# Kernel optimization log

Measured on AMD Instinct MI355X. Metric: run time of the kernel, lower is better.

## Reference

```python
import jax, jax.numpy as jnp
import numpy as np

B, N, D, H = 2, 2048, 1024, 16
DH = D // H
MASK_VALUE = -1e7


def setup_inputs() -> dict:
    key = jax.random.key(0)
    ks = jax.random.split(key, 8)
    scale = 0.02
    return {
        "queries": jax.random.normal(ks[0], (B, N, D), dtype=jnp.float32),
        "keys": jax.random.normal(ks[1], (B, N, D), dtype=jnp.float32),
        "values": jax.random.normal(ks[2], (B, N, D), dtype=jnp.float32),
        "valid_len": jax.random.randint(ks[3], (B * H,), 1, N + 1, dtype=jnp.int32),
        "Wq": jax.random.normal(ks[4], (D, D), dtype=jnp.float32) * scale,
        "Wk": jax.random.normal(ks[5], (D, D), dtype=jnp.float32) * scale,
        "Wv": jax.random.normal(ks[6], (D, D), dtype=jnp.float32) * scale,
        "Wo": jax.random.normal(ks[7], (D, D), dtype=jnp.float32) * scale,
    }


def reference(queries, keys, values, valid_len, Wq, Wk, Wv, Wo):
    b, n, d = queries.shape
    h, dh = H, d // H

    def split_heads(x):  # (b, n, d) -> (b, h, n, dh)
        return x.reshape(b, n, h, dh).transpose(0, 2, 1, 3)

    q = split_heads(queries @ Wq)
    k = split_heads(keys @ Wk)
    v = split_heads(values @ Wv)

    # (b, h, nq, nk) full score tensor, as in the original naive bmm path
    scores = jnp.einsum("bhqd,bhkd->bhqk", q, k) / jnp.sqrt(jnp.float32(dh))

    # valid_len is 1-D of length b*h; repeat_interleave over queries means the
    # mask depends only on the key index: keep k < valid_len[bh]
    vl = valid_len.reshape(b, h, 1, 1)
    keep = jnp.arange(n)[None, None, None, :] < vl  # (b, h, 1, nk)
    scores = jnp.where(keep, scores, MASK_VALUE)

    attn = jax.nn.softmax(scores, axis=-1)
    heads = jnp.einsum("bhqk,bhkd->bhqd", attn, v)  # (b, h, n, dh)
    out = heads.transpose(0, 2, 1, 3).reshape(b, n, d) @ Wo
    return out
```

## Files before the change

kernel.cpp:

```cpp
#include <hip/hip_runtime.h>

#define B_ 2
#define N_ 2048
#define D_ 1024
#define H_ 16
#define DH_ 64

typedef _Float16 half8 __attribute__((ext_vector_type(8)));
typedef _Float16 half4 __attribute__((ext_vector_type(4)));
typedef float f32x4 __attribute__((ext_vector_type(4)));

__device__ __forceinline__ void gl2lds16(const _Float16* g, _Float16* l) {
  __builtin_amdgcn_global_load_lds(
      (const __attribute__((address_space(1))) void*)g,
      (__attribute__((address_space(3))) void*)l, 16, 0, 0);
}

__global__ __launch_bounds__(256) void convert_x_kernel(
    const float* __restrict__ q, const float* __restrict__ k,
    const float* __restrict__ v, _Float16* __restrict__ dst) {
  const float* s = (blockIdx.y == 0) ? q : (blockIdx.y == 1) ? k : v;
  _Float16* d = dst + (size_t)blockIdx.y * ((size_t)B_ * N_ * D_);
  size_t idx = ((size_t)blockIdx.x * 256 + threadIdx.x) * 8;
  float4 a = *(const float4*)(s + idx);
  float4 b = *(const float4*)(s + idx + 4);
  half8 h;
  h[0] = (_Float16)a.x; h[1] = (_Float16)a.y; h[2] = (_Float16)a.z; h[3] = (_Float16)a.w;
  h[4] = (_Float16)b.x; h[5] = (_Float16)b.y; h[6] = (_Float16)b.z; h[7] = (_Float16)b.w;
  *(half8*)(d + idx) = h;
}

__global__ __launch_bounds__(256) void convert_w_kernel(
    const float* __restrict__ Wq, const float* __restrict__ Wk,
    const float* __restrict__ Wv, const float* __restrict__ Wo,
    _Float16* __restrict__ WtAll) {
  const float* W = (blockIdx.z == 0) ? Wq : (blockIdx.z == 1) ? Wk
                  : (blockIdx.z == 2) ? Wv : Wo;
  _Float16* Wt = WtAll + (size_t)blockIdx.z * D_ * D_;
  __shared__ float tile[64][65];
  int k0 = blockIdx.y * 64, n0 = blockIdx.x * 64;
  int tr = threadIdx.x >> 4, tc = threadIdx.x & 15;
#pragma unroll
  for (int i = 0; i < 4; ++i) {
    int r = tr + i * 16;
    float4 va = *(const float4*)(W + (size_t)(k0 + r) * D_ + n0 + tc * 4);
    tile[r][tc * 4 + 0] = va.x; tile[r][tc * 4 + 1] = va.y;
    tile[r][tc * 4 + 2] = va.z; tile[r][tc * 4 + 3] = va.w;
  }
  __syncthreads();
#pragma unroll
  for (int i = 0; i < 4; ++i) {
    int r = tr + i * 16;
    half4 hv;
    hv[0] = (_Float16)tile[tc * 4 + 0][r];
    hv[1] = (_Float16)tile[tc * 4 + 1][r];
    hv[2] = (_Float16)tile[tc * 4 + 2][r];
    hv[3] = (_Float16)tile[tc * 4 + 3][r];
    *(half4*)(Wt + (size_t)(n0 + r) * D_ + k0 + tc * 4) = hv;
  }
}

#define BK 32

template <int NT, int MODE>
__global__ __launch_bounds__(256) void gemm_f16_kernel(
    const _Float16* __restrict__ Aall, const _Float16* __restrict__ Btall,
    _Float16* __restrict__ ChAll, float* __restrict__ Cf32) {
  constexpr int BN = NT * 32;
  constexpr int K = D_;
  __shared__ __attribute__((aligned(16))) _Float16 As[128 * BK];
  __shared__ __attribute__((aligned(16))) _Float16 Bs[BN * BK];
  const int z = blockIdx.z;
  const _Float16* A  = Aall  + (size_t)z * ((size_t)B_ * N_ * D_);
  const _Float16* Bt = Btall + (size_t)z * ((size_t)D_ * D_);
  _Float16* Chead = ChAll + (size_t)z * ((size_t)B_ * N_ * D_);

  const int tid = threadIdx.x;
  const int m0 = blockIdx.y * 128, n0 = blockIdx.x * BN;
  const int lane = tid & 63, w = tid >> 6;
  const int quad = lane >> 4, l15 = lane & 15;
  const int wm = (w >> 1) * 64, wn = (w & 1) * (BN / 2);
  const int swz = (quad ^ ((l15 >> 1) & 3)) * 8;
  f32x4 acc[4][NT] = {};

  for (int kt = 0; kt < K; kt += BK) {
    if (kt) __syncthreads();
#pragma unroll
    for (int p = 0; p < 2; ++p) {
      int c = p * 256 + tid;
      int row = c >> 2, pg = c & 3;
      int gl = pg ^ ((row >> 1) & 3);
      gl2lds16(A + (size_t)(m0 + row) * K + kt + gl * 8, &As[c * 8]);
    }
#pragma unroll
    for (int p = 0; p < NT / 2; ++p) {
      int c = p * 256 + tid;
      int row = c >> 2, pg = c & 3;
      int gl = pg ^ ((row >> 1) & 3);
      gl2lds16(Bt + (size_t)(n0 + row) * K + kt + gl * 8, &Bs[c * 8]);
    }
    __syncthreads();
    half8 af[4], bf[NT];
#pragma unroll
    for (int mt = 0; mt < 4; ++mt)
      af[mt] = *(const half8*)&As[(wm + mt * 16 + l15) * 32 + swz];
#pragma unroll
    for (int nt = 0; nt < NT; ++nt)
      bf[nt] = *(const half8*)&Bs[(wn + nt * 16 + l15) * 32 + swz];
#pragma unroll
    for (int mt = 0; mt < 4; ++mt)
#pragma unroll
      for (int nt = 0; nt < NT; ++nt)
        acc[mt][nt] = __builtin_amdgcn_mfma_f32_16x16x32_f16(
            af[mt], bf[nt], acc[mt][nt], 0, 0, 0);
  }

#pragma unroll
  for (int mt = 0; mt < 4; ++mt) {
    int mrow = m0 + wm + mt * 16 + quad * 4;
#pragma unroll
    for (int nt = 0; nt < NT; ++nt) {
      int jcol = n0 + wn + nt * 16 + l15;
#pragma unroll
      for (int r = 0; r < 4; ++r) {
        float val = acc[mt][nt][r];
        int m = mrow + r;
        if (MODE == 0) {
          int b = m >> 11, n = m & (N_ - 1);
          int h = jcol >> 6, dh = jcol & (DH_ - 1);
          Chead[((((size_t)(b * H_ + h)) * N_ + n) * DH_) + dh] = (_Float16)val;
        } else {
          Cf32[(size_t)m * D_ + jcol] = val;
        }
      }
    }
  }
}

__global__ __launch_bounds__(256, 4) void attn_kernel(
    const _Float16* __restrict__ Qh, const _Float16* __restrict__ Kh,
    const _Float16* __restrict__ Vh, const int* __restrict__ vlen,
    _Float16* __restrict__ Hd) {
  __shared__ __attribute__((aligned(16))) _Float16 Ks[2][64 * 64];
  __shared__ __attribute__((aligned(16))) _Float16 Vt[2][64 * 64];
  const int bh = blockIdx.x, q0 = blockIdx.y * 64;
  const int b = bh >> 4, h = bh & (H_ - 1);
  const int vl = vlen[bh];
  const int tid = threadIdx.x, lane = tid & 63, w = tid >> 6;
  const int quad = lane >> 4, l15 = lane & 15;
  const _Float16* Qb = Qh + (size_t)bh * N_ * DH_;
  const _Float16* Kb = Kh + (size_t)bh * N_ * DH_;
  const _Float16* Vb = Vh + (size_t)bh * N_ * DH_;
  const int KT = (vl + 63) >> 6;

  const half8 qb0 = *(const half8*)(Qb + (size_t)(q0 + w * 16 + l15) * DH_ + quad * 8);
  const half8 qb1 = *(const half8*)(Qb + (size_t)(q0 + w * 16 + l15) * DH_ + 32 + quad * 8);

  half8 kpre[2], vpre[2];
  auto prefetch = [&](int k0) {
#pragma unroll
    for (int p = 0; p < 2; ++p) {
      int c = p * 256 + tid;
      int row = c >> 3, pg = c & 7, g = pg ^ (row & 7);
      kpre[p] = *(const half8*)(Kb + (size_t)(k0 + row) * DH_ + g * 8);
      vpre[p] = *(const half8*)(Vb + (size_t)(k0 + lane) * DH_ + (w + p * 4) * 8);
    }
  };
  auto commit = [&](int buf) {
#pragma unroll
    for (int p = 0; p < 2; ++p) {
      int c = p * 256 + tid;
      *(half8*)&Ks[buf][c * 8] = kpre[p];
      int dhg = w + p * 4;
#pragma unroll
      for (int u = 0; u < 8; ++u) {
        int dh = dhg * 8 + u;
        Vt[buf][dh * 64 + (((lane >> 2) ^ (dh & 15)) << 2) + (lane & 3)] = vpre[p][u];
      }
    }
  };

  prefetch(0);
  commit(0);
  if (KT > 1) prefetch(64);
  __syncthreads();

  const int sw  = (quad ^ (l15 & 7)) * 8;
  const int sw2 = ((quad + 4) ^ (l15 & 7)) * 8;
  const float sc2 = 0.125f * 1.44269504088896f;
  const half4 ones = {(_Float16)1, (_Float16)1, (_Float16)1, (_Float16)1};
  f32x4 Oacc[4] = {};
  f32x4 lacc = {};

  for (int kt = 0; kt < KT; ++kt) {
    const int cur = kt & 1;
    if (kt + 1 < KT) commit(1 - cur);
    if (kt + 2 < KT) prefetch((kt + 2) * 64);

    f32x4 s[4];
#pragma unroll
    for (int nt = 0; nt < 4; ++nt) {
      int r = nt * 16 + l15;
      half8 ka0 = *(const half8*)&Ks[cur][r * 64 + sw];
      half8 ka1 = *(const half8*)&Ks[cur][r * 64 + sw2];
      f32x4 c = {};
      c = __builtin_amdgcn_mfma_f32_16x16x32_f16(ka0, qb0, c, 0, 0, 0);
      c = __builtin_amdgcn_mfma_f32_16x16x32_f16(ka1, qb1, c, 0, 0, 0);
      s[nt] = c;
    }
    const int k0 = kt * 64;
    half4 pf[4];
    if (k0 + 64 <= vl) {
#pragma unroll
      for (int nt = 0; nt < 4; ++nt)
#pragma unroll
        for (int r = 0; r < 4; ++r)
          pf[nt][r] = (_Float16)exp2f(s[nt][r] * sc2);
    } else {
#pragma unroll
      for (int nt = 0; nt < 4; ++nt) {
        int keyb = k0 + nt * 16 + quad * 4;
#pragma unroll
        for (int r = 0; r < 4; ++r) {
          float p = exp2f(s[nt][r] * sc2);
          pf[nt][r] = (keyb + r < vl) ? (_Float16)p : (_Float16)0.f;
        }
      }
    }
#pragma unroll
    for (int nt = 0; nt < 4; ++nt) {
      lacc = __builtin_amdgcn_mfma_f32_16x16x16f16(ones, pf[nt], lacc, 0, 0, 0);
#pragma unroll
      for (int dt = 0; dt < 4; ++dt) {
        int dh = dt * 16 + l15;
        half4 va = *(const half4*)&Vt[cur][dh * 64 + (((nt * 4 + quad) ^ l15) << 2)];
        Oacc[dt] = __builtin_amdgcn_mfma_f32_16x16x16f16(va, pf[nt], Oacc[dt], 0, 0, 0);
      }
    }
    __syncthreads();
  }

  float inv_l = 1.0f / lacc[0];
  int q = q0 + w * 16 + l15;
  _Float16* out = Hd + ((size_t)(b * N_ + q)) * D_ + h * DH_;
#pragma unroll
  for (int dt = 0; dt < 4; ++dt) {
    half4 o;
#pragma unroll
    for (int r = 0; r < 4; ++r) o[r] = (_Float16)(Oacc[dt][r] * inv_l);
    *(half4*)(out + dt * 16 + quad * 4) = o;
  }
}

extern "C" void kernel_launch(void* const* d_in, const int* in_sizes, int n_in,
                              void* d_out, int out_size, void* d_ws, size_t ws_size,
                              hipStream_t stream) {
  const float* q  = (const float*)d_in[0];
  const float* k  = (const float*)d_in[1];
  const float* v  = (const float*)d_in[2];
  const int*   vl = (const int*)d_in[3];
  const float* Wq = (const float*)d_in[4];
  const float* Wk = (const float*)d_in[5];
  const float* Wv = (const float*)d_in[6];
  const float* Wo = (const float*)d_in[7];

  const size_t XSZ = (size_t)B_ * N_ * D_;
  const size_t WSZ = (size_t)D_ * D_;
  _Float16* ws = (_Float16*)d_ws;
  _Float16* Xf = ws;
  _Float16* Wt = Xf + 3 * XSZ;
  _Float16* Qh = Wt + 4 * WSZ;
  _Float16* Hd = Qh + 3 * XSZ;

  convert_x_kernel<<<dim3(2048, 3), 256, 0, stream>>>(q, k, v, Xf);
  convert_w_kernel<<<dim3(16, 16, 4), 256, 0, stream>>>(Wq, Wk, Wv, Wo, Wt);

  gemm_f16_kernel<4, 0><<<dim3(D_ / 128, 32, 3), 256, 0, stream>>>(
      Xf, Wt, Qh, nullptr);

  attn_kernel<<<dim3(B_ * H_, N_ / 64), 256, 0, stream>>>(
      Qh, Qh + XSZ, Qh + 2 * XSZ, vl, Hd);

  gemm_f16_kernel<2, 1><<<dim3(D_ / 64, 32, 1), 256, 0, stream>>>(
      Hd, Wt + 3 * WSZ, nullptr, (float*)d_out);
}
```

Baseline: 243.3 us.

## Add persistent LPT-scheduled attention, pre-transposed V, and BK=64 GEMM tiles

Attention becomes a persistent kernel: 512 blocks pull work items from an atomic counter, and heads are ordered longest-valid-length first by a small sort kernel. This aims to balance the uneven per-head work that comes from variable valid_len. A separate kernel pre-transposes V in global memory so the attention LDS commit uses vectorized half4 stores instead of scalar scatter stores. The GEMM K-tile is doubled to 64 with a new XOR swizzle, halving the number of barriers per K loop. The cost is two extra launches, an atomic per work item, and more LDS per GEMM block, which may lower occupancy.

```diff
diff --git a/kernel.cpp b/kernel.cpp
--- a/kernel.cpp
+++ b/kernel.cpp
@@ -5,6 +5,7 @@
 #define D_ 1024
 #define H_ 16
 #define DH_ 64
+#define NITEMS 1024
 
 typedef _Float16 half8 __attribute__((ext_vector_type(8)));
 typedef _Float16 half4 __attribute__((ext_vector_type(4)));
@@ -60,16 +61,14 @@
   }
 }
 
-#define BK 32
-
 template <int NT, int MODE>
 __global__ __launch_bounds__(256) void gemm_f16_kernel(
     const _Float16* __restrict__ Aall, const _Float16* __restrict__ Btall,
     _Float16* __restrict__ ChAll, float* __restrict__ Cf32) {
   constexpr int BN = NT * 32;
   constexpr int K = D_;
-  __shared__ __attribute__((aligned(16))) _Float16 As[128 * BK];
-  __shared__ __attribute__((aligned(16))) _Float16 Bs[BN * BK];
+  __shared__ __attribute__((aligned(16))) _Float16 As[128 * 64];
+  __shared__ __attribute__((aligned(16))) _Float16 Bs[BN * 64];
   const int z = blockIdx.z;
   const _Float16* A  = Aall  + (size_t)z * ((size_t)B_ * N_ * D_);
   const _Float16* Bt = Btall + (size_t)z * ((size_t)D_ * D_);
@@ -80,39 +79,47 @@
   const int lane = tid & 63, w = tid >> 6;
   const int quad = lane >> 4, l15 = lane & 15;
   const int wm = (w >> 1) * 64, wn = (w & 1) * (BN / 2);
-  const int swz = (quad ^ ((l15 >> 1) & 3)) * 8;
+  const int l7 = l15 & 7;
   f32x4 acc[4][NT] = {};
 
-  for (int kt = 0; kt < K; kt += BK) {
+  for (int kt = 0; kt < K; kt += 64) {
     if (kt) __syncthreads();
 #pragma unroll
-    for (int p = 0; p < 2; ++p) {
+    for (int p = 0; p < 4; ++p) {
       int c = p * 256 + tid;
-      int row = c >> 2, pg = c & 3;
-      int gl = pg ^ ((row >> 1) & 3);
+      int row = c >> 3, pg = c & 7, gl = pg ^ (row & 7);
       gl2lds16(A + (size_t)(m0 + row) * K + kt + gl * 8, &As[c * 8]);
     }
 #pragma unroll
-    for (int p = 0; p < NT / 2; ++p) {
+    for (int p = 0; p < NT; ++p) {
       int c = p * 256 + tid;
-      int row = c >> 2, pg = c & 3;
-      int gl = pg ^ ((row >> 1) & 3);
+      int row = c >> 3, pg = c & 7, gl = pg ^ (row & 7);
       gl2lds16(Bt + (size_t)(n0 + row) * K + kt + gl * 8, &Bs[c * 8]);
     }
     __syncthreads();
-    half8 af[4], bf[NT];
-#pragma unroll
-    for (int mt = 0; mt < 4; ++mt)
-      af[mt] = *(const half8*)&As[(wm + mt * 16 + l15) * 32 + swz];
-#pragma unroll
-    for (int nt = 0; nt < NT; ++nt)
-      bf[nt] = *(const half8*)&Bs[(wn + nt * 16 + l15) * 32 + swz];
-#pragma unroll
-    for (int mt = 0; mt < 4; ++mt)
-#pragma unroll
-      for (int nt = 0; nt < NT; ++nt)
-        acc[mt][nt] = __builtin_amdgcn_mfma_f32_16x16x32_f16(
-            af[mt], bf[nt], acc[mt][nt], 0, 0, 0);
+    half8 af[4][2], bf[NT][2];
+#pragma unroll
+    for (int mt = 0; mt < 4; ++mt) {
+      int row = wm + mt * 16 + l15;
+#pragma unroll
+      for (int hh = 0; hh < 2; ++hh)
+        af[mt][hh] = *(const half8*)&As[row * 64 + (((quad + 4 * hh) ^ l7) * 8)];
+    }
+#pragma unroll
+    for (int nt = 0; nt < NT; ++nt) {
+      int row = wn + nt * 16 + l15;
+#pragma unroll
+      for (int hh = 0; hh < 2; ++hh)
+        bf[nt][hh] = *(const half8*)&Bs[row * 64 + (((quad + 4 * hh) ^ l7) * 8)];
+    }
+#pragma unroll
+    for (int hh = 0; hh < 2; ++hh)
+#pragma unroll
+      for (int mt = 0; mt < 4; ++mt)
+#pragma unroll
+        for (int nt = 0; nt < NT; ++nt)
+          acc[mt][nt] = __builtin_amdgcn_mfma_f32_16x16x32_f16(
+              af[mt][hh], bf[nt][hh], acc[mt][nt], 0, 0, 0);
   }
 
 #pragma unroll
@@ -137,118 +144,167 @@
   }
 }
 
+__global__ __launch_bounds__(256) void transpose_v_kernel(
+    const _Float16* __restrict__ Vh, _Float16* __restrict__ VtG) {
+  __shared__ float Ls[64][65];
+  int bh = blockIdx.y, k0 = blockIdx.x * 64;
+  int tid = threadIdx.x;
+  const _Float16* src = Vh + (size_t)bh * N_ * DH_;
+#pragma unroll
+  for (int p = 0; p < 2; ++p) {
+    int c = p * 256 + tid, row = c >> 3, pg = c & 7;
+    half8 hv = *(const half8*)(src + (size_t)(k0 + row) * DH_ + pg * 8);
+#pragma unroll
+    for (int u = 0; u < 8; ++u) Ls[row][pg * 8 + u] = (float)hv[u];
+  }
+  __syncthreads();
+  _Float16* dst = VtG + (size_t)bh * N_ * DH_;
+#pragma unroll
+  for (int p = 0; p < 2; ++p) {
+    int c = p * 256 + tid, dh = c >> 3, pg = c & 7;
+    half8 hv;
+#pragma unroll
+    for (int u = 0; u < 8; ++u) hv[u] = (_Float16)Ls[pg * 8 + u][dh];
+    *(half8*)(dst + (size_t)dh * N_ + k0 + pg * 8) = hv;
+  }
+}
+
+__global__ void sort_heads_kernel(const int* __restrict__ vlen,
+                                  int* __restrict__ order, int* __restrict__ ctr) {
+  int i = threadIdx.x;
+  if (i == 0) *ctr = 0;
+  if (i < B_ * H_) {
+    int vi = vlen[i], rank = 0;
+    for (int j = 0; j < B_ * H_; ++j) {
+      int vj = vlen[j];
+      if (vj > vi || (vj == vi && j < i)) ++rank;
+    }
+    order[rank] = i;
+  }
+}
+
 __global__ __launch_bounds__(256, 4) void attn_kernel(
     const _Float16* __restrict__ Qh, const _Float16* __restrict__ Kh,
-    const _Float16* __restrict__ Vh, const int* __restrict__ vlen,
-    _Float16* __restrict__ Hd) {
+    const _Float16* __restrict__ VtG, const int* __restrict__ vlen,
+    _Float16* __restrict__ Hd, const int* __restrict__ order,
+    int* __restrict__ ctr) {
   __shared__ __attribute__((aligned(16))) _Float16 Ks[2][64 * 64];
   __shared__ __attribute__((aligned(16))) _Float16 Vt[2][64 * 64];
-  const int bh = blockIdx.x, q0 = blockIdx.y * 64;
-  const int b = bh >> 4, h = bh & (H_ - 1);
-  const int vl = vlen[bh];
+  __shared__ int sh_item;
   const int tid = threadIdx.x, lane = tid & 63, w = tid >> 6;
   const int quad = lane >> 4, l15 = lane & 15;
-  const _Float16* Qb = Qh + (size_t)bh * N_ * DH_;
-  const _Float16* Kb = Kh + (size_t)bh * N_ * DH_;
-  const _Float16* Vb = Vh + (size_t)bh * N_ * DH_;
-  const int KT = (vl + 63) >> 6;
-
-  const half8 qb0 = *(const half8*)(Qb + (size_t)(q0 + w * 16 + l15) * DH_ + quad * 8);
-  const half8 qb1 = *(const half8*)(Qb + (size_t)(q0 + w * 16 + l15) * DH_ + 32 + quad * 8);
-
-  half8 kpre[2], vpre[2];
-  auto prefetch = [&](int k0) {
-#pragma unroll
-    for (int p = 0; p < 2; ++p) {
-      int c = p * 256 + tid;
-      int row = c >> 3, pg = c & 7, g = pg ^ (row & 7);
-      kpre[p] = *(const half8*)(Kb + (size_t)(k0 + row) * DH_ + g * 8);
-      vpre[p] = *(const half8*)(Vb + (size_t)(k0 + lane) * DH_ + (w + p * 4) * 8);
-    }
-  };
-  auto commit = [&](int buf) {
-#pragma unroll
-    for (int p = 0; p < 2; ++p) {
-      int c = p * 256 + tid;
-      *(half8*)&Ks[buf][c * 8] = kpre[p];
-      int dhg = w + p * 4;
-#pragma unroll
-      for (int u = 0; u < 8; ++u) {
-        int dh = dhg * 8 + u;
-        Vt[buf][dh * 64 + (((lane >> 2) ^ (dh & 15)) << 2) + (lane & 3)] = vpre[p][u];
-      }
-    }
-  };
-
-  prefetch(0);
-  commit(0);
-  if (KT > 1) prefetch(64);
-  __syncthreads();
-
   const int sw  = (quad ^ (l15 & 7)) * 8;
   const int sw2 = ((quad + 4) ^ (l15 & 7)) * 8;
   const float sc2 = 0.125f * 1.44269504088896f;
   const half4 ones = {(_Float16)1, (_Float16)1, (_Float16)1, (_Float16)1};
-  f32x4 Oacc[4] = {};
-  f32x4 lacc = {};
-
-  for (int kt = 0; kt < KT; ++kt) {
-    const int cur = kt & 1;
-    if (kt + 1 < KT) commit(1 - cur);
-    if (kt + 2 < KT) prefetch((kt + 2) * 64);
-
-    f32x4 s[4];
-#pragma unroll
-    for (int nt = 0; nt < 4; ++nt) {
-      int r = nt * 16 + l15;
-      half8 ka0 = *(const half8*)&Ks[cur][r * 64 + sw];
-      half8 ka1 = *(const half8*)&Ks[cur][r * 64 + sw2];
-      f32x4 c = {};
-      c = __builtin_amdgcn_mfma_f32_16x16x32_f16(ka0, qb0, c, 0, 0, 0);
-      c = __builtin_amdgcn_mfma_f32_16x16x32_f16(ka1, qb1, c, 0, 0, 0);
-      s[nt] = c;
-    }
-    const int k0 = kt * 64;
-    half4 pf[4];
-    if (k0 + 64 <= vl) {
-#pragma unroll
-      for (int nt = 0; nt < 4; ++nt)
-#pragma unroll
-        for (int r = 0; r < 4; ++r)
-          pf[nt][r] = (_Float16)exp2f(s[nt][r] * sc2);
-    } else {
+
+  while (true) {
+    if (tid == 0) sh_item = atomicAdd(ctr, 1);
+    __syncthreads();
+    const int item = sh_item;
+    if (item >= NITEMS) return;
+    const int bh = order[item >> 5];
+    const int q0 = (item & 31) * 64;
+    const int b = bh >> 4, h = bh & (H_ - 1);
+    const int vl = vlen[bh];
+    const int KT = (vl + 63) >> 6;
+    const _Float16* Qb = Qh  + (size_t)bh * N_ * DH_;
+    const _Float16* Kb = Kh  + (size_t)bh * N_ * DH_;
+    const _Float16* Vb = VtG + (size_t)bh * N_ * DH_;
+
+    const half8 qb0 = *(const half8*)(Qb + (size_t)(q0 + w * 16 + l15) * DH_ + quad * 8);
+    const half8 qb1 = *(const half8*)(Qb + (size_t)(q0 + w * 16 + l15) * DH_ + 32 + quad * 8);
+
+    half8 kpre[2], vpre[2];
+    auto prefetch = [&](int k0k) {
+#pragma unroll
+      for (int p = 0; p < 2; ++p) {
+        int c = p * 256 + tid;
+        int row = c >> 3, pg = c & 7;
+        kpre[p] = *(const half8*)(Kb + (size_t)(k0k + row) * DH_ + (pg ^ (row & 7)) * 8);
+        vpre[p] = *(const half8*)(Vb + (size_t)row * N_ + k0k + pg * 8);
+      }
+    };
+    auto commit = [&](int buf) {
+#pragma unroll
+      for (int p = 0; p < 2; ++p) {
+        int c = p * 256 + tid;
+        int row = c >> 3, pg = c & 7;
+        *(half8*)&Ks[buf][c * 8] = kpre[p];
+        int j0 = (pg * 2) ^ (row & 15), j1 = (pg * 2 + 1) ^ (row & 15);
+        half4 lo = {vpre[p][0], vpre[p][1], vpre[p][2], vpre[p][3]};
+        half4 hi = {vpre[p][4], vpre[p][5], vpre[p][6], vpre[p][7]};
+        *(half4*)&Vt[buf][row * 64 + j0 * 4] = lo;
+        *(half4*)&Vt[buf][row * 64 + j1 * 4] = hi;
+      }
+    };
+
+    prefetch(0);
+    commit(0);
+    if (KT > 1) prefetch(64);
+    __syncthreads();
+
+    f32x4 Oacc[4] = {};
+    f32x4 lacc = {};
+
+    for (int kt = 0; kt < KT; ++kt) {
+      const int cur = kt & 1;
+      if (kt + 1 < KT) commit(1 - cur);
+      if (kt + 2 < KT) prefetch((kt + 2) * 64);
+
+      f32x4 s[4];
 #pragma unroll
       for (int nt = 0; nt < 4; ++nt) {
-        int keyb = k0 + nt * 16 + quad * 4;
-#pragma unroll
-        for (int r = 0; r < 4; ++r) {
-          float p = exp2f(s[nt][r] * sc2);
-          pf[nt][r] = (keyb + r < vl) ? (_Float16)p : (_Float16)0.f;
+        int r = nt * 16 + l15;
+        half8 ka0 = *(const half8*)&Ks[cur][r * 64 + sw];
+        half8 ka1 = *(const half8*)&Ks[cur][r * 64 + sw2];
+        f32x4 c = {};
+        c = __builtin_amdgcn_mfma_f32_16x16x32_f16(ka0, qb0, c, 0, 0, 0);
+        c = __builtin_amdgcn_mfma_f32_16x16x32_f16(ka1, qb1, c, 0, 0, 0);
+        s[nt] = c;
+      }
+      const int k0k = kt * 64;
+      half4 pf[4];
+      if (k0k + 64 <= vl) {
+#pragma unroll
+        for (int nt = 0; nt < 4; ++nt)
+#pragma unroll
+          for (int r = 0; r < 4; ++r)
+            pf[nt][r] = (_Float16)exp2f(s[nt][r] * sc2);
+      } else {
+#pragma unroll
+        for (int nt = 0; nt < 4; ++nt) {
+          int keyb = k0k + nt * 16 + quad * 4;
+#pragma unroll
+          for (int r = 0; r < 4; ++r) {
+            float p = exp2f(s[nt][r] * sc2);
+            pf[nt][r] = (keyb + r < vl) ? (_Float16)p : (_Float16)0.f;
+          }
         }
       }
-    }
-#pragma unroll
-    for (int nt = 0; nt < 4; ++nt) {
-      lacc = __builtin_amdgcn_mfma_f32_16x16x16f16(ones, pf[nt], lacc, 0, 0, 0);
-#pragma unroll
-      for (int dt = 0; dt < 4; ++dt) {
-        int dh = dt * 16 + l15;
-        half4 va = *(const half4*)&Vt[cur][dh * 64 + (((nt * 4 + quad) ^ l15) << 2)];
-        Oacc[dt] = __builtin_amdgcn_mfma_f32_16x16x16f16(va, pf[nt], Oacc[dt], 0, 0, 0);
-      }
-    }
-    __syncthreads();
-  }
-
-  float inv_l = 1.0f / lacc[0];
-  int q = q0 + w * 16 + l15;
-  _Float16* out = Hd + ((size_t)(b * N_ + q)) * D_ + h * DH_;
-#pragma unroll
-  for (int dt = 0; dt < 4; ++dt) {
-    half4 o;
-#pragma unroll
-    for (int r = 0; r < 4; ++r) o[r] = (_Float16)(Oacc[dt][r] * inv_l);
-    *(half4*)(out + dt * 16 + quad * 4) = o;
+#pragma unroll
+      for (int nt = 0; nt < 4; ++nt) {
+        lacc = __builtin_amdgcn_mfma_f32_16x16x16f16(ones, pf[nt], lacc, 0, 0, 0);
+#pragma unroll
+        for (int dt = 0; dt < 4; ++dt) {
+          int dh = dt * 16 + l15;
+          half4 va = *(const half4*)&Vt[cur][dh * 64 + (((nt * 4 + quad) ^ l15) << 2)];
+          Oacc[dt] = __builtin_amdgcn_mfma_f32_16x16x16f16(va, pf[nt], Oacc[dt], 0, 0, 0);
+        }
+      }
+      __syncthreads();
+    }
+
+    float inv_l = 1.0f / lacc[0];
+    int q = q0 + w * 16 + l15;
+    _Float16* out = Hd + ((size_t)(b * N_ + q)) * D_ + h * DH_;
+#pragma unroll
+    for (int dt = 0; dt < 4; ++dt) {
+      half4 o;
+#pragma unroll
+      for (int r = 0; r < 4; ++r) o[r] = (_Float16)(Oacc[dt][r] * inv_l);
+      *(half4*)(out + dt * 16 + quad * 4) = o;
+    }
   }
 }
 
@@ -271,6 +327,9 @@
   _Float16* Wt = Xf + 3 * XSZ;
   _Float16* Qh = Wt + 4 * WSZ;
   _Float16* Hd = Qh + 3 * XSZ;
+  int* ctr   = (int*)(Hd + XSZ);
+  int* order = ctr + 1;
+  _Float16* VtG = Xf;
 
   convert_x_kernel<<<dim3(2048, 3), 256, 0, stream>>>(q, k, v, Xf);
   convert_w_kernel<<<dim3(16, 16, 4), 256, 0, stream>>>(Wq, Wk, Wv, Wo, Wt);
@@ -278,8 +337,12 @@
   gemm_f16_kernel<4, 0><<<dim3(D_ / 128, 32, 3), 256, 0, stream>>>(
       Xf, Wt, Qh, nullptr);
 
-  attn_kernel<<<dim3(B_ * H_, N_ / 64), 256, 0, stream>>>(
-      Qh, Qh + XSZ, Qh + 2 * XSZ, vl, Hd);
+  transpose_v_kernel<<<dim3(N_ / 64, B_ * H_), 256, 0, stream>>>(
+      Qh + 2 * XSZ, VtG);
+  sort_heads_kernel<<<1, 64, 0, stream>>>(vl, order, ctr);
+
+  attn_kernel<<<dim3(512), 256, 0, stream>>>(
+      Qh, Qh + XSZ, VtG, vl, Hd, order, ctr);
 
   gemm_f16_kernel<2, 1><<<dim3(D_ / 64, 32, 1), 256, 0, stream>>>(
       Hd, Wt + 3 * WSZ, nullptr, (float*)d_out);
```

New measurement: 241.5 us. Within noise of the previous version (-0.7%).
